# Kernel tuning notes

Hardware: AMD Instinct MI355X
Metric: run time of the kernel (lower is better)

Reference implementation:

```python
import jax, jax.numpy as jnp
import numpy as np

D_MODEL = 2048
N_HEADS = 4
IDX_DIM = 64
B, TQ, TK = 2, 4096, 4096


def setup_inputs() -> dict:
    key = jax.random.key(0)
    k1, k2, k3, k4, k5 = jax.random.split(key, 5)
    x_q = jax.random.normal(k1, (B, TQ, D_MODEL), dtype=jnp.float32)
    x_k = jax.random.normal(k2, (B, TK, D_MODEL), dtype=jnp.float32)
    scale = 1.0 / np.sqrt(D_MODEL)
    Wq = jax.random.normal(k3, (D_MODEL, N_HEADS * IDX_DIM), dtype=jnp.float32) * scale
    Ww = jax.random.normal(k4, (D_MODEL, N_HEADS), dtype=jnp.float32) * scale
    Wk = jax.random.normal(k5, (D_MODEL, IDX_DIM), dtype=jnp.float32) * scale
    return {"x_q": x_q, "x_k": x_k, "Wq": Wq, "Ww": Ww, "Wk": Wk}


def reference(x_q, x_k, Wq, Ww, Wk):
    Bq, Tq, _ = x_q.shape
    # q_I: (B, Tq, H, d_idx); w_I: (B, Tq, H); k_I: (B, Tk, d_idx)
    q_I = (x_q @ Wq).reshape(Bq, Tq, N_HEADS, IDX_DIM)
    w_I = x_q @ Ww
    k_I = x_k @ Wk
    # per-head dot scores: (B, H, Tq, Tk), key projection shared across heads
    dot = jnp.einsum("bqhd,bkd->bhqk", q_I, k_I)
    activated = jax.nn.relu(dot)
    # weighted sum over heads -> (B, Tq, Tk)
    index_scores = jnp.einsum("bhqk,bqh->bqk", activated, w_I)
    return index_scores
```

## Files before the change

kernel.cpp:

```cpp
#include <hip/hip_runtime.h>
#include <hip/hip_bf16.h>

#define DM 2048
#define NH 4
#define DI 64
#define TQS 4096
#define TKS 4096
#define BB 2

typedef __attribute__((ext_vector_type(4))) float f32x4;
typedef __attribute__((ext_vector_type(8))) short bf16x8;

typedef __attribute__((address_space(1))) const void gvoid;
typedef __attribute__((address_space(3))) void lvoid;

__device__ __forceinline__ short f2bf(float f) {
  __hip_bfloat16 h = __float2bfloat16(f);
  return __builtin_bit_cast(short, h);
}

__device__ __forceinline__ bf16x8 cvt8(f32x4 a, f32x4 b) {
  bf16x8 r;
  r[0] = f2bf(a[0]); r[1] = f2bf(a[1]); r[2] = f2bf(a[2]); r[3] = f2bf(a[3]);
  r[4] = f2bf(b[0]); r[5] = f2bf(b[1]); r[6] = f2bf(b[2]); r[7] = f2bf(b[3]);
  return r;
}

__global__ __launch_bounds__(256) void transpose_qw(const float* __restrict__ Wq,
                                                    const float* __restrict__ Ww,
                                                    short* __restrict__ WT) {
  int idx = blockIdx.x * 256 + threadIdx.x;
  int n = idx >> 11, k = idx & 2047;
  float v = 0.f;
  if (n < 256) v = Wq[(size_t)k * 256 + n];
  else if (n < 260) v = Ww[(size_t)k * 4 + (n - 256)];
  WT[idx] = f2bf(v);
}

__global__ __launch_bounds__(256) void transpose_k(const float* __restrict__ Wk,
                                                   short* __restrict__ WT) {
  int idx = blockIdx.x * 256 + threadIdx.x;
  int n = idx >> 11, k = idx & 2047;
  WT[idx] = f2bf(Wk[(size_t)k * 64 + n]);
}

template <int NJ, bool QP>
__device__ __forceinline__ void proj_body(const float* __restrict__ X,
                                          const short* __restrict__ WT,
                                          short* __restrict__ O,
                                          float* __restrict__ wI, int blk,
                                          float* As ) {
  const int tid = threadIdx.x;
  const int wave = tid >> 6, lane = tid & 63;
  const int l15 = lane & 15, quad = lane >> 4;
  const int m0 = blk * 32;
  const int ldo = QP ? 256 : 64;

  int jt[NJ];
#pragma unroll
  for (int jj = 0; jj < NJ; ++jj) jt[jj] = QP ? (jj < 4 ? jj * 4 + wave : 16 + wave) : wave;

  const short* wb[NJ];
#pragma unroll
  for (int jj = 0; jj < NJ; ++jj) wb[jj] = WT + (size_t)(jt[jj] * 16 + l15) * DM + quad * 8;

  const int srow = tid >> 4;
  const int schunk = (tid & 15) ^ srow;
  const float* s0 = X + (size_t)(m0 + srow) * DM + schunk * 4;
  const float* s1 = X + (size_t)(m0 + 16 + srow) * DM + schunk * 4;
  const int d0 = tid * 16;
  const int d1 = 4096 + tid * 16;

  const f32x4 z = {0.f, 0.f, 0.f, 0.f};
  f32x4 acc[NJ][2];
#pragma unroll
  for (int jj = 0; jj < NJ; ++jj)
#pragma unroll
    for (int i = 0; i < 2; ++i) acc[jj][i] = z;

  char* lbase = (char*)As;

  __builtin_amdgcn_global_load_lds((gvoid*)s0, (lvoid*)(lbase + d0), 16, 0, 0);
  __builtin_amdgcn_global_load_lds((gvoid*)s1, (lvoid*)(lbase + d1), 16, 0, 0);
  __syncthreads();

  int cur = 0;
#pragma unroll 2
  for (int t = 0; t < 32; ++t) {
    bf16x8 bbv[NJ][2];
#pragma unroll
    for (int jj = 0; jj < NJ; ++jj)
#pragma unroll
      for (int ks = 0; ks < 2; ++ks)
        bbv[jj][ks] = *(const bf16x8*)(wb[jj] + t * 64 + ks * 32);
    __builtin_amdgcn_sched_barrier(0);

    if (t < 31) {
      const float* g0 = s0 + (t + 1) * 64;
      const float* g1 = s1 + (t + 1) * 64;
      char* l = lbase + (cur ^ 1) * 8192;
      __builtin_amdgcn_global_load_lds((gvoid*)g0, (lvoid*)(l + d0), 16, 0, 0);
      __builtin_amdgcn_global_load_lds((gvoid*)g1, (lvoid*)(l + d1), 16, 0, 0);
    }
    __builtin_amdgcn_sched_barrier(0);

    const float* Ab = As + cur * 2048;
    bf16x8 abf[2][2];
#pragma unroll
    for (int i = 0; i < 2; ++i)
#pragma unroll
      for (int ks = 0; ks < 2; ++ks) {
        const int rb = (i * 16 + l15) * 64;
        const int cg = ks * 8 + quad * 2;
        f32x4 a0 = *(const f32x4*)(Ab + rb + ((cg ^ l15) << 2));
        f32x4 a1 = *(const f32x4*)(Ab + rb + (((cg + 1) ^ l15) << 2));
        abf[i][ks] = cvt8(a0, a1);
      }

#pragma unroll
    for (int jj = 0; jj < NJ; ++jj)
#pragma unroll
      for (int i = 0; i < 2; ++i)
#pragma unroll
        for (int ks = 0; ks < 2; ++ks)
          acc[jj][i] = __builtin_amdgcn_mfma_f32_16x16x32_bf16(abf[i][ks], bbv[jj][ks],
                                                               acc[jj][i], 0, 0, 0);

    __syncthreads();
    cur ^= 1;
  }

#pragma unroll
  for (int jj = 0; jj < NJ; ++jj) {
    if (QP && jt[jj] >= 16) {
      if (jt[jj] == 16 && l15 < 4) {
#pragma unroll
        for (int i = 0; i < 2; ++i)
#pragma unroll
          for (int r = 0; r < 4; ++r)
            wI[(size_t)(m0 + i * 16 + quad * 4 + r) * NH + l15] = acc[jj][i][r];
      }
    } else {
#pragma unroll
      for (int i = 0; i < 2; ++i)
#pragma unroll
        for (int r = 0; r < 4; ++r)
          O[(size_t)(m0 + i * 16 + quad * 4 + r) * ldo + jt[jj] * 16 + l15] =
              f2bf(acc[jj][i][r]);
    }
  }
}

__global__ __launch_bounds__(256, 2) void proj_fused(const float* __restrict__ xq,
                                                     const float* __restrict__ xk,
                                                     const short* __restrict__ WqwT,
                                                     const short* __restrict__ WkT,
                                                     short* __restrict__ qb,
                                                     short* __restrict__ kb,
                                                     float* __restrict__ wIb) {
  __shared__ __align__(16) float As[2][2048];
  if (blockIdx.x < 256)
    proj_body<5, true>(xq, WqwT, qb, wIb, blockIdx.x, &As[0][0]);
  else
    proj_body<1, false>(xk, WkT, kb, nullptr, blockIdx.x - 256, &As[0][0]);
}

__global__ __launch_bounds__(256, 2) void score_kernel(const short* __restrict__ qb,
                                                       const short* __restrict__ kb,
                                                       const float* __restrict__ wI,
                                                       float* __restrict__ out) {
  const int b = blockIdx.z;
  const int qt = blockIdx.y;
  const int kt = blockIdx.x;
  const int tid = threadIdx.x;
  const int wave = tid >> 6, lane = tid & 63;
  const int wm = wave >> 1, wn = wave & 1;
  const int l15 = lane & 15, quad = lane >> 4;

  bf16x8 bf[4][2];
  {
    const short* kbase =
        kb + (size_t)(b * TKS + kt * 128 + wn * 64 + l15) * DI + quad * 8;
#pragma unroll
    for (int j = 0; j < 4; ++j)
#pragma unroll
      for (int ks = 0; ks < 2; ++ks)
        bf[j][ks] = *(const bf16x8*)(kbase + j * 16 * DI + ks * 32);
  }

  const f32x4 z = {0.f, 0.f, 0.f, 0.f};
  f32x4 facc[4][4];
#pragma unroll
  for (int i = 0; i < 4; ++i)
#pragma unroll
    for (int j = 0; j < 4; ++j) facc[i][j] = z;

  const short* qbase =
      qb + (size_t)(b * TQS + qt * 128 + wm * 64 + l15) * (NH * DI) + quad * 8;
  const float* wbase = wI + (size_t)(b * TQS + qt * 128 + wm * 64 + quad * 4) * NH;

  bf16x8 af[2][4][2];
#pragma unroll
  for (int i = 0; i < 4; ++i)
#pragma unroll
    for (int ks = 0; ks < 2; ++ks)
      af[0][i][ks] = *(const bf16x8*)(qbase + i * 16 * (NH * DI) + ks * 32);

#pragma unroll
  for (int h = 0; h < NH; ++h) {
    if (h < NH - 1) {
#pragma unroll
      for (int i = 0; i < 4; ++i)
#pragma unroll
        for (int ks = 0; ks < 2; ++ks)
          af[(h + 1) & 1][i][ks] =
              *(const bf16x8*)(qbase + (h + 1) * DI + i * 16 * (NH * DI) + ks * 32);
    }

    f32x4 acc[4][4];
#pragma unroll
    for (int i = 0; i < 4; ++i)
#pragma unroll
      for (int j = 0; j < 4; ++j) acc[i][j] = z;

#pragma unroll
    for (int ks = 0; ks < 2; ++ks)
#pragma unroll
      for (int i = 0; i < 4; ++i)
#pragma unroll
        for (int j = 0; j < 4; ++j)
          acc[i][j] = __builtin_amdgcn_mfma_f32_16x16x32_bf16(
              af[h & 1][i][ks], bf[j][ks], acc[i][j], 0, 0, 0);

#pragma unroll
    for (int i = 0; i < 4; ++i) {
      float wv[4];
#pragma unroll
      for (int r = 0; r < 4; ++r) wv[r] = wbase[(i * 16 + r) * NH + h];
#pragma unroll
      for (int j = 0; j < 4; ++j)
#pragma unroll
        for (int r = 0; r < 4; ++r)
          facc[i][j][r] += wv[r] * fmaxf(acc[i][j][r], 0.f);
    }
  }

  float* obase = out + (size_t)b * TQS * TKS +
                 (size_t)(qt * 128 + wm * 64 + quad * 4) * TKS + kt * 128 + wn * 64 + l15;
#pragma unroll
  for (int i = 0; i < 4; ++i)
#pragma unroll
    for (int r = 0; r < 4; ++r)
#pragma unroll
      for (int j = 0; j < 4; ++j)
        __builtin_nontemporal_store(facc[i][j][r],
                                    &obase[(size_t)(i * 16 + r) * TKS + j * 16]);
}

extern "C" void kernel_launch(void* const* d_in, const int* in_sizes, int n_in,
                              void* d_out, int out_size, void* d_ws, size_t ws_size,
                              hipStream_t stream) {
  const float* x_q = (const float*)d_in[0];
  const float* x_k = (const float*)d_in[1];
  const float* Wq  = (const float*)d_in[2];
  const float* Ww  = (const float*)d_in[3];
  const float* Wk  = (const float*)d_in[4];
  float* out = (float*)d_out;

  char* ws = (char*)d_ws;
  short* qbuf = (short*)(ws);
  short* kbuf = (short*)(ws + (4u << 20));
  float* wIb  = (float*)(ws + (5u << 20));
  short* WqwT = (short*)(ws + (5u << 20) + (128u << 10));
  short* WkT  = (short*)(ws + (7u << 20));

  transpose_qw<<<(320 * 2048) / 256, 256, 0, stream>>>(Wq, Ww, WqwT);
  transpose_k<<<(64 * 2048) / 256, 256, 0, stream>>>(Wk, WkT);

  proj_fused<<<512, 256, 0, stream>>>(x_q, x_k, WqwT, WkT, qbuf, kbuf, wIb);

  score_kernel<<<dim3(TKS / 128, TQS / 128, BB), 256, 0, stream>>>(qbuf, kbuf, wIb, out);
}
```

Measured before the change: 301.6 us.

## Deepen projection pipeline to a 4-slot LDS ring with prefetched weights

The fused projection kernel's two-buffer LDS scheme becomes a 4-slot ring with three activation tiles kept in flight. The bf16 weight fragments are now double-buffered in registers one step ahead. The main loop drops __syncthreads in favour of raw s_barrier plus an explicit prologue vmcnt wait, and is followed by a manually peeled epilogue. The aim is to hide global-memory latency in the projection stage, at the cost of twice the LDS, more registers, and reliance on implicit waitcnt ordering for the async LDS loads.

After: 305.0 us. No clear change (+1.1%).

```diff
diff --git a/kernel.cpp b/kernel.cpp
--- a/kernel.cpp
+++ b/kernel.cpp
@@ -55,6 +55,7 @@
   const int l15 = lane & 15, quad = lane >> 4;
   const int m0 = blk * 32;
   const int ldo = QP ? 256 : 64;
+  constexpr int NB = NJ * 2;
 
   int jt[NJ];
 #pragma unroll
@@ -68,8 +69,24 @@
   const int schunk = (tid & 15) ^ srow;
   const float* s0 = X + (size_t)(m0 + srow) * DM + schunk * 4;
   const float* s1 = X + (size_t)(m0 + 16 + srow) * DM + schunk * 4;
-  const int d0 = tid * 16;
-  const int d1 = 4096 + tid * 16;
+  const int d0 = tid * 16, d1 = 4096 + tid * 16;
+  char* lb = (char*)As;
+
+#pragma unroll
+  for (int s = 0; s < 3; ++s) {
+    __builtin_amdgcn_global_load_lds((gvoid*)(s0 + s * 64), (lvoid*)(lb + s * 8192 + d0), 16, 0, 0);
+    __builtin_amdgcn_global_load_lds((gvoid*)(s1 + s * 64), (lvoid*)(lb + s * 8192 + d1), 16, 0, 0);
+  }
+  bf16x8 bb[2][NJ][2];
+#pragma unroll
+  for (int jj = 0; jj < NJ; ++jj)
+#pragma unroll
+    for (int ks = 0; ks < 2; ++ks)
+      bb[0][jj][ks] = *(const bf16x8*)(wb[jj] + ks * 32);
+  __builtin_amdgcn_sched_barrier(0);
+  asm volatile("s_waitcnt vmcnt(%0)" ::"i"(4 + NB));
+  __builtin_amdgcn_sched_barrier(0);
+  __builtin_amdgcn_s_barrier();
 
   const f32x4 z = {0.f, 0.f, 0.f, 0.f};
   f32x4 acc[NJ][2];
@@ -78,32 +95,19 @@
 #pragma unroll
     for (int i = 0; i < 2; ++i) acc[jj][i] = z;
 
-  char* lbase = (char*)As;
-
-  __builtin_amdgcn_global_load_lds((gvoid*)s0, (lvoid*)(lbase + d0), 16, 0, 0);
-  __builtin_amdgcn_global_load_lds((gvoid*)s1, (lvoid*)(lbase + d1), 16, 0, 0);
-  __syncthreads();
-
-  int cur = 0;
-#pragma unroll 2
-  for (int t = 0; t < 32; ++t) {
-    bf16x8 bbv[NJ][2];
+  auto loadB = [&](int t1, int bbi) {
 #pragma unroll
     for (int jj = 0; jj < NJ; ++jj)
 #pragma unroll
       for (int ks = 0; ks < 2; ++ks)
-        bbv[jj][ks] = *(const bf16x8*)(wb[jj] + t * 64 + ks * 32);
-    __builtin_amdgcn_sched_barrier(0);
-
-    if (t < 31) {
-      const float* g0 = s0 + (t + 1) * 64;
-      const float* g1 = s1 + (t + 1) * 64;
-      char* l = lbase + (cur ^ 1) * 8192;
-      __builtin_amdgcn_global_load_lds((gvoid*)g0, (lvoid*)(l + d0), 16, 0, 0);
-      __builtin_amdgcn_global_load_lds((gvoid*)g1, (lvoid*)(l + d1), 16, 0, 0);
-    }
-    __builtin_amdgcn_sched_barrier(0);
-
+        bb[bbi][jj][ks] = *(const bf16x8*)(wb[jj] + t1 * 64 + ks * 32);
+  };
+  auto stage = [&](int t3) {
+    char* l = lb + (t3 & 3) * 8192;
+    __builtin_amdgcn_global_load_lds((gvoid*)(s0 + t3 * 64), (lvoid*)(l + d0), 16, 0, 0);
+    __builtin_amdgcn_global_load_lds((gvoid*)(s1 + t3 * 64), (lvoid*)(l + d1), 16, 0, 0);
+  };
+  auto compute = [&](int cur, int bbi) {
     const float* Ab = As + cur * 2048;
     bf16x8 abf[2][2];
 #pragma unroll
@@ -116,19 +120,47 @@
         f32x4 a1 = *(const f32x4*)(Ab + rb + (((cg + 1) ^ l15) << 2));
         abf[i][ks] = cvt8(a0, a1);
       }
-
 #pragma unroll
     for (int jj = 0; jj < NJ; ++jj)
 #pragma unroll
       for (int i = 0; i < 2; ++i)
 #pragma unroll
         for (int ks = 0; ks < 2; ++ks)
-          acc[jj][i] = __builtin_amdgcn_mfma_f32_16x16x32_bf16(abf[i][ks], bbv[jj][ks],
+          acc[jj][i] = __builtin_amdgcn_mfma_f32_16x16x32_bf16(abf[i][ks], bb[bbi][jj][ks],
                                                                acc[jj][i], 0, 0, 0);
-
-    __syncthreads();
-    cur ^= 1;
-  }
+  };
+
+#pragma unroll 4
+  for (int t = 0; t < 28; ++t) {
+    loadB(t + 1, (t + 1) & 1);
+    __builtin_amdgcn_sched_barrier(0);
+    stage(t + 3);
+    __builtin_amdgcn_sched_barrier(0);
+    compute(t & 3, t & 1);
+    __builtin_amdgcn_sched_barrier(0);
+    __builtin_amdgcn_s_barrier();
+  }
+  loadB(29, 1);
+  __builtin_amdgcn_sched_barrier(0);
+  stage(31);
+  __builtin_amdgcn_sched_barrier(0);
+  compute(0, 0);
+  __builtin_amdgcn_sched_barrier(0);
+  __builtin_amdgcn_s_barrier();
+
+  loadB(30, 0);
+  __builtin_amdgcn_sched_barrier(0);
+  compute(1, 1);
+  __builtin_amdgcn_sched_barrier(0);
+  __builtin_amdgcn_s_barrier();
+
+  loadB(31, 1);
+  __builtin_amdgcn_sched_barrier(0);
+  compute(2, 0);
+  __builtin_amdgcn_sched_barrier(0);
+  __builtin_amdgcn_s_barrier();
+
+  compute(3, 1);
 
 #pragma unroll
   for (int jj = 0; jj < NJ; ++jj) {
@@ -158,7 +190,7 @@
                                                      short* __restrict__ qb,
                                                      short* __restrict__ kb,
                                                      float* __restrict__ wIb) {
-  __shared__ __align__(16) float As[2][2048];
+  __shared__ __align__(16) float As[4][2048];
   if (blockIdx.x < 256)
     proj_body<5, true>(xq, WqwT, qb, wIb, blockIdx.x, &As[0][0]);
   else
```

## Split projection block rows across 8 waves instead of 4

Applied to the files above, without the earlier changes.

The projection kernel now runs 512 threads per block. Each wave handles one 16-row half of the 32-row tile (wr) and one column group (wc), so each wave holds half the accumulators and does half the MFMAs per step. Each thread now issues a single global-to-LDS load per stage instead of two. The aim is more waves in flight and lower per-wave register pressure for a proj stage that is memory bound. In exchange, each B-operand (weight) fragment is now loaded by twice as many waves, and the block-wide barriers cover more threads.

New measurement: 335.1 us. 11.1% more time.

```diff
diff --git a/kernel.cpp b/kernel.cpp
--- a/kernel.cpp
+++ b/kernel.cpp
@@ -52,36 +52,31 @@
                                           float* As ) {
   const int tid = threadIdx.x;
   const int wave = tid >> 6, lane = tid & 63;
+  const int wc = wave & 3, wr = wave >> 2;
   const int l15 = lane & 15, quad = lane >> 4;
   const int m0 = blk * 32;
   const int ldo = QP ? 256 : 64;
 
   int jt[NJ];
 #pragma unroll
-  for (int jj = 0; jj < NJ; ++jj) jt[jj] = QP ? (jj < 4 ? jj * 4 + wave : 16 + wave) : wave;
+  for (int jj = 0; jj < NJ; ++jj) jt[jj] = QP ? (jj < 4 ? jj * 4 + wc : 16 + wc) : wc;
 
   const short* wb[NJ];
 #pragma unroll
   for (int jj = 0; jj < NJ; ++jj) wb[jj] = WT + (size_t)(jt[jj] * 16 + l15) * DM + quad * 8;
 
   const int srow = tid >> 4;
-  const int schunk = (tid & 15) ^ srow;
+  const int schunk = (tid & 15) ^ (srow & 15);
   const float* s0 = X + (size_t)(m0 + srow) * DM + schunk * 4;
-  const float* s1 = X + (size_t)(m0 + 16 + srow) * DM + schunk * 4;
   const int d0 = tid * 16;
-  const int d1 = 4096 + tid * 16;
+  char* lb = (char*)As;
 
   const f32x4 z = {0.f, 0.f, 0.f, 0.f};
-  f32x4 acc[NJ][2];
-#pragma unroll
-  for (int jj = 0; jj < NJ; ++jj)
-#pragma unroll
-    for (int i = 0; i < 2; ++i) acc[jj][i] = z;
-
-  char* lbase = (char*)As;
-
-  __builtin_amdgcn_global_load_lds((gvoid*)s0, (lvoid*)(lbase + d0), 16, 0, 0);
-  __builtin_amdgcn_global_load_lds((gvoid*)s1, (lvoid*)(lbase + d1), 16, 0, 0);
+  f32x4 acc[NJ];
+#pragma unroll
+  for (int jj = 0; jj < NJ; ++jj) acc[jj] = z;
+
+  __builtin_amdgcn_global_load_lds((gvoid*)s0, (lvoid*)(lb + d0), 16, 0, 0);
   __syncthreads();
 
   int cur = 0;
@@ -95,36 +90,30 @@
         bbv[jj][ks] = *(const bf16x8*)(wb[jj] + t * 64 + ks * 32);
     __builtin_amdgcn_sched_barrier(0);
 
-    if (t < 31) {
-      const float* g0 = s0 + (t + 1) * 64;
-      const float* g1 = s1 + (t + 1) * 64;
-      char* l = lbase + (cur ^ 1) * 8192;
-      __builtin_amdgcn_global_load_lds((gvoid*)g0, (lvoid*)(l + d0), 16, 0, 0);
-      __builtin_amdgcn_global_load_lds((gvoid*)g1, (lvoid*)(l + d1), 16, 0, 0);
-    }
+    if (t < 31)
+      __builtin_amdgcn_global_load_lds((gvoid*)(s0 + (t + 1) * 64),
+                                       (lvoid*)(lb + (cur ^ 1) * 8192 + d0), 16, 0, 0);
     __builtin_amdgcn_sched_barrier(0);
 
     const float* Ab = As + cur * 2048;
-    bf16x8 abf[2][2];
-#pragma unroll
-    for (int i = 0; i < 2; ++i)
+    bf16x8 abf[2];
+    {
+      const int rb = (wr * 16 + l15) * 64;
 #pragma unroll
       for (int ks = 0; ks < 2; ++ks) {
-        const int rb = (i * 16 + l15) * 64;
         const int cg = ks * 8 + quad * 2;
         f32x4 a0 = *(const f32x4*)(Ab + rb + ((cg ^ l15) << 2));
         f32x4 a1 = *(const f32x4*)(Ab + rb + (((cg + 1) ^ l15) << 2));
-        abf[i][ks] = cvt8(a0, a1);
+        abf[ks] = cvt8(a0, a1);
       }
+    }
 
 #pragma unroll
     for (int jj = 0; jj < NJ; ++jj)
 #pragma unroll
-      for (int i = 0; i < 2; ++i)
-#pragma unroll
-        for (int ks = 0; ks < 2; ++ks)
-          acc[jj][i] = __builtin_amdgcn_mfma_f32_16x16x32_bf16(abf[i][ks], bbv[jj][ks],
-                                                               acc[jj][i], 0, 0, 0);
+      for (int ks = 0; ks < 2; ++ks)
+        acc[jj] = __builtin_amdgcn_mfma_f32_16x16x32_bf16(abf[ks], bbv[jj][ks],
+                                                          acc[jj], 0, 0, 0);
 
     __syncthreads();
     cur ^= 1;
@@ -135,23 +124,19 @@
     if (QP && jt[jj] >= 16) {
       if (jt[jj] == 16 && l15 < 4) {
 #pragma unroll
-        for (int i = 0; i < 2; ++i)
-#pragma unroll
-          for (int r = 0; r < 4; ++r)
-            wI[(size_t)(m0 + i * 16 + quad * 4 + r) * NH + l15] = acc[jj][i][r];
+        for (int r = 0; r < 4; ++r)
+          wI[(size_t)(m0 + wr * 16 + quad * 4 + r) * NH + l15] = acc[jj][r];
       }
     } else {
 #pragma unroll
-      for (int i = 0; i < 2; ++i)
-#pragma unroll
-        for (int r = 0; r < 4; ++r)
-          O[(size_t)(m0 + i * 16 + quad * 4 + r) * ldo + jt[jj] * 16 + l15] =
-              f2bf(acc[jj][i][r]);
-    }
-  }
-}
-
-__global__ __launch_bounds__(256, 2) void proj_fused(const float* __restrict__ xq,
+      for (int r = 0; r < 4; ++r)
+        O[(size_t)(m0 + wr * 16 + quad * 4 + r) * ldo + jt[jj] * 16 + l15] =
+            f2bf(acc[jj][r]);
+    }
+  }
+}
+
+__global__ __launch_bounds__(512, 4) void proj_fused(const float* __restrict__ xq,
                                                      const float* __restrict__ xk,
                                                      const short* __restrict__ WqwT,
                                                      const short* __restrict__ WkT,
@@ -277,7 +262,7 @@
   transpose_qw<<<(320 * 2048) / 256, 256, 0, stream>>>(Wq, Ww, WqwT);
   transpose_k<<<(64 * 2048) / 256, 256, 0, stream>>>(Wk, WkT);
 
-  proj_fused<<<512, 256, 0, stream>>>(x_q, x_k, WqwT, WkT, qbuf, kbuf, wIb);
+  proj_fused<<<512, 512, 0, stream>>>(x_q, x_k, WqwT, WkT, qbuf, kbuf, wIb);
 
   score_kernel<<<dim3(TKS / 128, TQS / 128, BB), 256, 0, stream>>>(qbuf, kbuf, wIb, out);
 }
```

## Deepen projection K-tile to 256 with double-buffered B register prefetch

Applied to the files above, without the earlier changes.

The projection kernel now stages 256-wide K slices of the fp32 activations into LDS per iteration instead of 64-wide, cutting the number of barriers from 32 to 8. Weight fragments are prefetched into two register buffers that alternate across four inner sub-steps, so global loads overlap with MFMA work. The cost is four times more LDS per block (64KB), which may limit occupancy at 2 blocks per CU, plus higher register pressure.

Result: slower. 312.0 us (+3.4%).

```diff
diff --git a/kernel.cpp b/kernel.cpp
--- a/kernel.cpp
+++ b/kernel.cpp
@@ -64,12 +64,26 @@
 #pragma unroll
   for (int jj = 0; jj < NJ; ++jj) wb[jj] = WT + (size_t)(jt[jj] * 16 + l15) * DM + quad * 8;
 
-  const int srow = tid >> 4;
-  const int schunk = (tid & 15) ^ srow;
-  const float* s0 = X + (size_t)(m0 + srow) * DM + schunk * 4;
-  const float* s1 = X + (size_t)(m0 + 16 + srow) * DM + schunk * 4;
-  const int d0 = tid * 16;
-  const int d1 = 4096 + tid * 16;
+  char* lb = (char*)As;
+
+  auto stage = [&](int tn, int buf) {
+#pragma unroll
+    for (int j = 0; j < 8; ++j) {
+      const int row = j * 4 + wave;
+      const float* src = X + (size_t)(m0 + row) * DM + tn * 256 + ((lane ^ (row & 15)) << 2);
+      char* dst = lb + buf * 32768 + (j * 256 + tid) * 16;
+      __builtin_amdgcn_global_load_lds((gvoid*)src, (lvoid*)dst, 16, 0, 0);
+    }
+  };
+
+  bf16x8 bbv[2][NJ][2];
+  auto loadB = [&](int k64, int p) {
+#pragma unroll
+    for (int jj = 0; jj < NJ; ++jj)
+#pragma unroll
+      for (int ks = 0; ks < 2; ++ks)
+        bbv[p][jj][ks] = *(const bf16x8*)(wb[jj] + k64 * 64 + ks * 32);
+  };
 
   const f32x4 z = {0.f, 0.f, 0.f, 0.f};
   f32x4 acc[NJ][2];
@@ -78,56 +92,52 @@
 #pragma unroll
     for (int i = 0; i < 2; ++i) acc[jj][i] = z;
 
-  char* lbase = (char*)As;
-
-  __builtin_amdgcn_global_load_lds((gvoid*)s0, (lvoid*)(lbase + d0), 16, 0, 0);
-  __builtin_amdgcn_global_load_lds((gvoid*)s1, (lvoid*)(lbase + d1), 16, 0, 0);
-  __syncthreads();
-
-  int cur = 0;
-#pragma unroll 2
-  for (int t = 0; t < 32; ++t) {
-    bf16x8 bbv[NJ][2];
-#pragma unroll
-    for (int jj = 0; jj < NJ; ++jj)
-#pragma unroll
-      for (int ks = 0; ks < 2; ++ks)
-        bbv[jj][ks] = *(const bf16x8*)(wb[jj] + t * 64 + ks * 32);
-    __builtin_amdgcn_sched_barrier(0);
-
-    if (t < 31) {
-      const float* g0 = s0 + (t + 1) * 64;
-      const float* g1 = s1 + (t + 1) * 64;
-      char* l = lbase + (cur ^ 1) * 8192;
-      __builtin_amdgcn_global_load_lds((gvoid*)g0, (lvoid*)(l + d0), 16, 0, 0);
-      __builtin_amdgcn_global_load_lds((gvoid*)g1, (lvoid*)(l + d1), 16, 0, 0);
-    }
-    __builtin_amdgcn_sched_barrier(0);
-
-    const float* Ab = As + cur * 2048;
+  auto computeKK = [&](int buf, int kk, int p) {
+    const float* Ab = As + buf * 8192;
     bf16x8 abf[2][2];
 #pragma unroll
-    for (int i = 0; i < 2; ++i)
+    for (int i = 0; i < 2; ++i) {
+      const int rb = (i * 16 + l15) * 256;
 #pragma unroll
       for (int ks = 0; ks < 2; ++ks) {
-        const int rb = (i * 16 + l15) * 64;
-        const int cg = ks * 8 + quad * 2;
+        const int cg = kk * 16 + ks * 8 + quad * 2;
         f32x4 a0 = *(const f32x4*)(Ab + rb + ((cg ^ l15) << 2));
         f32x4 a1 = *(const f32x4*)(Ab + rb + (((cg + 1) ^ l15) << 2));
         abf[i][ks] = cvt8(a0, a1);
       }
-
+    }
 #pragma unroll
     for (int jj = 0; jj < NJ; ++jj)
 #pragma unroll
       for (int i = 0; i < 2; ++i)
 #pragma unroll
         for (int ks = 0; ks < 2; ++ks)
-          acc[jj][i] = __builtin_amdgcn_mfma_f32_16x16x32_bf16(abf[i][ks], bbv[jj][ks],
+          acc[jj][i] = __builtin_amdgcn_mfma_f32_16x16x32_bf16(abf[i][ks], bbv[p][jj][ks],
                                                                acc[jj][i], 0, 0, 0);
-
+  };
+
+  stage(0, 0);
+  __syncthreads();
+
+#pragma unroll 2
+  for (int t = 0; t < 8; ++t) {
+    const int buf = t & 1;
+    loadB(t * 4 + 0, 0);
+    loadB(t * 4 + 1, 1);
+    __builtin_amdgcn_sched_barrier(0);
+    if (t < 7) stage(t + 1, buf ^ 1);
+    __builtin_amdgcn_sched_barrier(0);
+    computeKK(buf, 0, 0);
+    loadB(t * 4 + 2, 0);
+    __builtin_amdgcn_sched_barrier(0);
+    computeKK(buf, 1, 1);
+    loadB(t * 4 + 3, 1);
+    __builtin_amdgcn_sched_barrier(0);
+    computeKK(buf, 2, 0);
+    __builtin_amdgcn_sched_barrier(0);
+    computeKK(buf, 3, 1);
+    __builtin_amdgcn_sched_barrier(0);
     __syncthreads();
-    cur ^= 1;
   }
 
 #pragma unroll
@@ -158,7 +168,7 @@
                                                      short* __restrict__ qb,
                                                      short* __restrict__ kb,
                                                      float* __restrict__ wIb) {
-  __shared__ __align__(16) float As[2][2048];
+  __shared__ __align__(16) float As[2][8192];
   if (blockIdx.x < 256)
     proj_body<5, true>(xq, WqwT, qb, wIb, blockIdx.x, &As[0][0]);
   else
```
